# Performance work log

Hardware: AMD Instinct MI355X
Metric: run time of the kernel (lower is better)

The kernel has to match this reference:

```python
import jax, jax.numpy as jnp
import numpy as np

L, H, NH, HD, FF, S, B, V, NL = 2, 2048, 16, 128, 4096, 1024, 2, 32000, 4
R, SCALING, BLK = 2, 16.0 / 2.0, 64  # LoRA r=2, alpha=16 -> scaling 8; NF4 blocksize 64
NF4 = jnp.array([-1.0, -0.6961928009986877, -0.5250730514526367, -0.39491748809814453,
                 -0.28444138169288635, -0.18477343022823334, -0.09105003625154495, 0.0,
                 0.07958029955625534, 0.16093020141124725, 0.24611230194568634,
                 0.33791524171829224, 0.44070982933044434, 0.5626170039176941,
                 0.7229568362236023, 1.0], dtype=jnp.float32)

def dequant(codes, scales):
    # codes [out, in] int -> NF4 values; scales [out, in//BLK] absmax per 64-block
    return NF4[codes] * jnp.repeat(scales, BLK, axis=-1)

def qlin(x, codes, scales, A, Bm):
    # fused dequant + GEMM + LoRA low-rank update: x @ (Wd + s*B@A).T
    W = dequant(codes, scales)
    return x @ W.T + SCALING * ((x @ A.T) @ Bm.T)

def layer_norm(x, g, b):
    mu = jnp.mean(x, -1, keepdims=True)
    var = jnp.var(x, -1, keepdims=True)
    return (x - mu) * jax.lax.rsqrt(var + 1e-5) * g + b

def rope(x):  # x [B,S,NH,HD]
    half = HD // 2
    inv = 1.0 / (10000.0 ** (jnp.arange(half, dtype=jnp.float32) / half))
    ang = jnp.arange(S, dtype=jnp.float32)[:, None] * inv[None, :]
    cos = jnp.concatenate([jnp.cos(ang)] * 2, -1)[None, :, None, :]
    sin = jnp.concatenate([jnp.sin(ang)] * 2, -1)[None, :, None, :]
    x1, x2 = x[..., :half], x[..., half:]
    return x * cos + jnp.concatenate([-x2, x1], -1) * sin

def setup_inputs() -> dict:
    key = jax.random.key(0)
    it = iter(jax.random.split(key, 64))
    nrm = lambda shp, s: jax.random.normal(next(it), shp, jnp.float32) * s
    cod = lambda shp: jax.random.randint(next(it), shp, 0, 16, jnp.int32)
    scl = lambda shp: jax.random.uniform(next(it), shp, jnp.float32) * 0.02 + 1e-3
    lens = jax.random.randint(next(it), (B,), S // 2, S + 1)
    return dict(
        input_ids=jax.random.randint(next(it), (B, S), 0, V, jnp.int32),
        attention_mask=(jnp.arange(S)[None, :] < lens[:, None]).astype(jnp.int32),
        labels=jax.random.randint(next(it), (B,), 0, NL, jnp.int32),
        embed=nrm((V, H), 0.02),
        qkv_codes=cod((L, 3 * H, H)), qkv_scales=scl((L, 3 * H, H // BLK)),
        qkv_A=nrm((L, R, H), 0.01), qkv_B=nrm((L, 3 * H, R), 0.01),
        dense_codes=cod((L, H, H)), dense_scales=scl((L, H, H // BLK)),
        dense_A=nrm((L, R, H), 0.01), dense_B=nrm((L, H, R), 0.01),
        min_codes=cod((L, 2 * FF, H)), min_scales=scl((L, 2 * FF, H // BLK)),
        min_A=nrm((L, R, H), 0.01), min_B=nrm((L, 2 * FF, R), 0.01),
        mout_codes=cod((L, H, FF)), mout_scales=scl((L, H, FF // BLK)),
        mout_A=nrm((L, R, FF), 0.01), mout_B=nrm((L, H, R), 0.01),
        ln1_g=jnp.ones((L, H)), ln1_b=jnp.zeros((L, H)),
        ln2_g=jnp.ones((L, H)), ln2_b=jnp.zeros((L, H)),
        lnf_g=jnp.ones((H,)), lnf_b=jnp.zeros((H,)),
        classifier_w=nrm((NL, H), 0.01),
    )

def reference(input_ids, attention_mask, labels, embed, qkv_codes, qkv_scales, qkv_A, qkv_B,
              dense_codes, dense_scales, dense_A, dense_B, min_codes, min_scales, min_A, min_B,
              mout_codes, mout_scales, mout_A, mout_B, ln1_g, ln1_b, ln2_g, ln2_b,
              lnf_g, lnf_b, classifier_w):
    x = embed[input_ids]  # [B,S,H]
    mask = jnp.tril(jnp.ones((S, S), bool))[None, None] & (attention_mask[:, None, None, :] > 0)
    for l in range(L):
        h = layer_norm(x, ln1_g[l], ln1_b[l])
        qkv = qlin(h, qkv_codes[l], qkv_scales[l], qkv_A[l], qkv_B[l]).reshape(B, S, NH, 3 * HD)
        q, k, v = qkv[..., :HD], qkv[..., HD:2 * HD], qkv[..., 2 * HD:]
        q, k = rope(q), rope(k)
        scores = jnp.einsum('bqhd,bkhd->bhqk', q, k) / np.float32(np.sqrt(HD))
        probs = jax.nn.softmax(jnp.where(mask, scores, jnp.float32(-1e30)), -1)
        attn = jnp.einsum('bhqk,bkhd->bqhd', probs, v).reshape(B, S, H)
        x = x + qlin(attn, dense_codes[l], dense_scales[l], dense_A[l], dense_B[l])
        h2 = layer_norm(x, ln2_g[l], ln2_b[l])
        u = qlin(h2, min_codes[l], min_scales[l], min_A[l], min_B[l])  # [B,S,2*FF] packed SwiGLU
        g = jax.nn.silu(u[..., :FF]) * u[..., FF:]
        x = x + qlin(g, mout_codes[l], mout_scales[l], mout_A[l], mout_B[l])
    x = layer_norm(x, lnf_g, lnf_b)
    eos = x[jnp.arange(B), attention_mask.sum(1) - 1]  # last non-padded token hidden
    logits = eos @ classifier_w.T
    logp = jax.nn.log_softmax(logits, -1)
    loss = -jnp.mean(logp[jnp.arange(B), labels])
    return loss, logits
```

## Files before the change

kernel.cpp:

```cpp
#include <hip/hip_runtime.h>

typedef unsigned short u16;
typedef __attribute__((ext_vector_type(4))) float f32x4;
typedef __attribute__((ext_vector_type(8))) short short8;
typedef __attribute__((ext_vector_type(4))) short short4v;

constexpr int CL  = 2;
constexpr int CH  = 2048;
constexpr int CNH = 16;
constexpr int CHD = 128;
constexpr int CFF = 4096;
constexpr int CS  = 1024;
constexpr int CB  = 2;
constexpr int CNL = 4;
constexpr int CM  = CB * CS;
#define SCALING 8.0f

__device__ __constant__ float NF4TAB[16] = {
    -1.0f, -0.6961928009986877f, -0.5250730514526367f, -0.39491748809814453f,
    -0.28444138169288635f, -0.18477343022823334f, -0.09105003625154495f, 0.0f,
    0.07958029955625534f, 0.16093020141124725f, 0.24611230194568634f,
    0.33791524171829224f, 0.44070982933044434f, 0.5626170039176941f,
    0.7229568362236023f, 1.0f};

__device__ __forceinline__ u16 f2bf(float f) {
  union { float f; unsigned u; } v; v.f = f;
  unsigned r = v.u + 0x7fffu + ((v.u >> 16) & 1u);
  return (u16)(r >> 16);
}
__device__ __forceinline__ float bf2f(u16 u) {
  union { unsigned u; float f; } v; v.u = ((unsigned)u) << 16;
  return v.f;
}

__device__ __forceinline__ float blockReduceSum(float v) {
  __shared__ float sh[4];
  #pragma unroll
  for (int o = 32; o > 0; o >>= 1) v += __shfl_down(v, o);
  __syncthreads();
  if ((threadIdx.x & 63) == 0) sh[threadIdx.x >> 6] = v;
  __syncthreads();
  return sh[0] + sh[1] + sh[2] + sh[3];
}

__global__ void k_embed(const int* __restrict__ ids, const float* __restrict__ emb,
                        float* __restrict__ x) {
  int m = blockIdx.x;
  const float4* src = (const float4*)(emb + (size_t)ids[m] * CH);
  float4* dst = (float4*)(x + (size_t)m * CH);
  for (int i = threadIdx.x; i < CH / 4; i += 256) dst[i] = src[i];
}

__global__ void k_ln_xa(const float* __restrict__ x, const float* __restrict__ g,
                        const float* __restrict__ b, const float* __restrict__ A,
                        u16* __restrict__ o, float* __restrict__ xA) {
  int m = blockIdx.x, tid = threadIdx.x;
  const float* row = x + (size_t)m * CH;
  float s = 0.f, s2 = 0.f;
  for (int i = tid; i < CH / 4; i += 256) {
    float4 v = ((const float4*)row)[i];
    s += v.x + v.y + v.z + v.w;
    s2 += v.x * v.x + v.y * v.y + v.z * v.z + v.w * v.w;
  }
  s = blockReduceSum(s);
  s2 = blockReduceSum(s2);
  float mu = s / CH, var = s2 / CH - mu * mu;
  float rs = rsqrtf(var + 1e-5f);
  u16* orow = o + (size_t)m * CH;
  float s0 = 0.f, s1 = 0.f;
  for (int i = tid; i < CH / 4; i += 256) {
    float4 v = ((const float4*)row)[i];
    float4 gv = ((const float4*)g)[i];
    float4 bv = ((const float4*)b)[i];
    float4 a0 = ((const float4*)A)[i];
    float4 a1 = ((const float4*)(A + CH))[i];
    float h0 = (v.x - mu) * rs * gv.x + bv.x;
    float h1 = (v.y - mu) * rs * gv.y + bv.y;
    float h2 = (v.z - mu) * rs * gv.z + bv.z;
    float h3 = (v.w - mu) * rs * gv.w + bv.w;
    short4v ov = { (short)f2bf(h0), (short)f2bf(h1), (short)f2bf(h2), (short)f2bf(h3) };
    *(short4v*)(orow + i * 4) = ov;
    s0 += h0 * a0.x + h1 * a0.y + h2 * a0.z + h3 * a0.w;
    s1 += h0 * a1.x + h1 * a1.y + h2 * a1.z + h3 * a1.w;
  }
  s0 = blockReduceSum(s0);
  s1 = blockReduceSum(s1);
  if (tid == 0) { xA[2 * m] = s0; xA[2 * m + 1] = s1; }
}

__global__ void k_xa(const u16* __restrict__ xb, const float* __restrict__ A,
                     float* __restrict__ xA, int K) {
  int m = blockIdx.x, tid = threadIdx.x;
  const u16* row = xb + (size_t)m * K;
  float s0 = 0.f, s1 = 0.f;
  for (int c = tid; c < K / 8; c += 256) {
    short8 v = *(const short8*)(row + c * 8);
    #pragma unroll
    for (int e = 0; e < 8; ++e) {
      float f = bf2f((u16)v[e]);
      s0 += f * A[c * 8 + e];
      s1 += f * A[K + c * 8 + e];
    }
  }
  s0 = blockReduceSum(s0);
  s1 = blockReduceSum(s1);
  if (tid == 0) { xA[2 * m] = s0; xA[2 * m + 1] = s1; }
}

__global__ void k_dequant(const int* __restrict__ codes, const float* __restrict__ scales,
                          u16* __restrict__ w, int kshift, long total) {
  __shared__ float lut[16];
  if (threadIdx.x < 16) lut[threadIdx.x] = NF4TAB[threadIdx.x];
  __syncthreads();
  long base = ((long)blockIdx.x * 256 + threadIdx.x) * 8;
  if (base >= total) return;
  long n = base >> kshift;
  int k = (int)(base & ((1L << kshift) - 1));
  float sc = scales[(size_t)n * (1 << (kshift - 6)) + (k >> 6)];
  const int* cp = codes + base;
  short8 o;
  #pragma unroll
  for (int i = 0; i < 8; ++i) o[i] = (short)f2bf(lut[cp[i] & 15] * sc);
  *(short8*)(w + base) = o;
}

__global__ void k_ropetab(float* __restrict__ cosT, float* __restrict__ sinT) {
  int i = blockIdx.x * 256 + threadIdx.x;
  if (i >= CS * 64) return;
  int s = i >> 6, d = i & 63;
  float inv = powf(10000.0f, -(float)d / 64.0f);
  float a = (float)s * inv;
  cosT[i] = cosf(a);
  sinT[i] = sinf(a);
}

__global__ void k_rope(const u16* __restrict__ qkv, const float* __restrict__ cosT,
                       const float* __restrict__ sinT, u16* __restrict__ Qb,
                       u16* __restrict__ Kb) {
  int bid = blockIdx.x;
  int s = bid & (CS - 1);
  int z = bid >> 10;
  int b = z >> 4, h = z & 15;
  int d = threadIdx.x;
  const u16* base = qkv + ((size_t)(b * CS + s)) * (3 * CH) + h * (3 * CHD);
  int dh = d & 63;
  float c = cosT[s * 64 + dh], sn = sinT[s * 64 + dh];
  float sgn = (d < 64) ? -1.0f : 1.0f;
  float q = bf2f(base[d]),       qp = bf2f(base[d ^ 64]);
  float k = bf2f(base[CHD + d]), kp = bf2f(base[CHD + (d ^ 64)]);
  size_t oi = ((size_t)z * CS + s) * CHD + d;
  Qb[oi] = f2bf(q * c + sgn * qp * sn);
  Kb[oi] = f2bf(k * c + sgn * kp * sn);
}

__global__ void k_vtrans(const u16* __restrict__ qkv, u16* __restrict__ Vt) {
  __shared__ u16 tile[32][33];
  int z = blockIdx.z;
  int b = z >> 4, h = z & 15;
  int s0 = blockIdx.x * 32, d0 = blockIdx.y * 32;
  int tx = threadIdx.x, ty = threadIdx.y;
  #pragma unroll
  for (int i = 0; i < 32; i += 8)
    tile[ty + i][tx] =
        qkv[((size_t)(b * CS + s0 + ty + i)) * (3 * CH) + h * (3 * CHD) + 2 * CHD + d0 + tx];
  __syncthreads();
  #pragma unroll
  for (int i = 0; i < 32; i += 8)
    Vt[((size_t)z * CHD + d0 + ty + i) * CS + s0 + tx] = tile[tx][ty + i];
}

__global__ __launch_bounds__(256, 2) void k_flash(
    const u16* __restrict__ Qb, const u16* __restrict__ Kb, const u16* __restrict__ Vt,
    const int* __restrict__ amask, u16* __restrict__ out) {
  __shared__ u16 Ks[64 * 128];
  __shared__ u16 Vs[128 * 64];
  __shared__ float bias[CS];
  __shared__ u16 Ps[4][16][80];
  int bid = blockIdx.x;
  int qt = 15 - (bid >> 5);
  int z = bid & 31;
  int b = z >> 4, h = z & 15;
  int tid = threadIdx.x, lane = tid & 63, wid = tid >> 6;
  int lrow = lane & 15, lgrp = lane >> 4;
  const u16* Qz = Qb + (size_t)z * CS * CHD;
  const u16* Kz = Kb + (size_t)z * CS * CHD;
  const u16* Vz = Vt + (size_t)z * CHD * CS;

  for (int i = tid; i < CS; i += 256)
    bias[i] = amask[b * CS + i] ? 0.f : -1e30f;

  int qrow = qt * 64 + wid * 16 + lrow;
  short8 qf[4];
  #pragma unroll
  for (int kk = 0; kk < 4; ++kk)
    qf[kk] = *(const short8*)(Qz + (size_t)qrow * CHD + kk * 32 + lgrp * 8);

  float m_r[4], l_r[4];
  #pragma unroll
  for (int r = 0; r < 4; ++r) { m_r[r] = -3e38f; l_r[r] = 0.f; }
  f32x4 o_acc[8];
  #pragma unroll
  for (int dj = 0; dj < 8; ++dj) o_acc[dj] = (f32x4){0.f, 0.f, 0.f, 0.f};

  const float SCL = 0.08838834764831845f;

  for (int t = 0; t <= qt; ++t) {
    int k0 = t * 64;
    __syncthreads();
    #pragma unroll
    for (int it = 0; it < 4; ++it) {
      int c = it * 256 + tid;
      int key = c >> 4, ch = c & 15;
      short8 v = *(const short8*)(Kz + (size_t)(k0 + key) * CHD + ch * 8);
      *(short8*)((char*)Ks + key * 256 + ((ch * 16) ^ ((key & 7) << 4))) = v;
    }
    #pragma unroll
    for (int it = 0; it < 4; ++it) {
      int c = it * 256 + tid;
      int d = c >> 3, ch = c & 7;
      short8 v = *(const short8*)(Vz + (size_t)d * CS + k0 + ch * 8);
      *(short8*)((char*)Vs + d * 128 + ((ch * 16) ^ ((d & 7) << 4))) = v;
    }
    __syncthreads();

    f32x4 s_acc[4];
    #pragma unroll
    for (int nj = 0; nj < 4; ++nj) s_acc[nj] = (f32x4){0.f, 0.f, 0.f, 0.f};
    #pragma unroll
    for (int kk = 0; kk < 4; ++kk) {
      #pragma unroll
      for (int nj = 0; nj < 4; ++nj) {
        int key = nj * 16 + lrow;
        short8 kf = *(const short8*)((const char*)Ks + key * 256 +
                                     (((kk * 32 + lgrp * 8) * 2) ^ ((key & 7) << 4)));
        s_acc[nj] = __builtin_amdgcn_mfma_f32_16x16x32_bf16(qf[kk], kf, s_acc[nj], 0, 0, 0);
      }
    }

    bool diag = (t == qt);
    float p[4][4], mx[4];
    #pragma unroll
    for (int r = 0; r < 4; ++r) {
      int ql = wid * 16 + 4 * lgrp + r;
      float rm = -3e38f;
      #pragma unroll
      for (int nj = 0; nj < 4; ++nj) {
        int kl = nj * 16 + lrow;
        float v = s_acc[nj][r] * SCL + bias[k0 + kl];
        if (diag && kl > ql) v = -1e30f;
        p[nj][r] = v;
        rm = fmaxf(rm, v);
      }
      mx[r] = rm;
    }
    #pragma unroll
    for (int o = 1; o < 16; o <<= 1)
      #pragma unroll
      for (int r = 0; r < 4; ++r) mx[r] = fmaxf(mx[r], __shfl_xor(mx[r], o));
    float ps[4], alpha[4];
    #pragma unroll
    for (int r = 0; r < 4; ++r) {
      float mn = fmaxf(m_r[r], mx[r]);
      alpha[r] = __expf(m_r[r] - mn);
      m_r[r] = mn;
      float acc = 0.f;
      #pragma unroll
      for (int nj = 0; nj < 4; ++nj) {
        float e = __expf(p[nj][r] - mn);
        p[nj][r] = e;
        acc += e;
      }
      ps[r] = acc;
    }
    #pragma unroll
    for (int o = 1; o < 16; o <<= 1)
      #pragma unroll
      for (int r = 0; r < 4; ++r) ps[r] += __shfl_xor(ps[r], o);
    #pragma unroll
    for (int r = 0; r < 4; ++r) {
      l_r[r] = l_r[r] * alpha[r] + ps[r];
      #pragma unroll
      for (int dj = 0; dj < 8; ++dj) o_acc[dj][r] *= alpha[r];
    }

    #pragma unroll
    for (int r = 0; r < 4; ++r)
      #pragma unroll
      for (int nj = 0; nj < 4; ++nj)
        Ps[wid][4 * lgrp + r][nj * 16 + lrow] = f2bf(p[nj][r]);
    #pragma unroll
    for (int kk2 = 0; kk2 < 2; ++kk2) {
      short8 pa = *(const short8*)(&Ps[wid][lrow][kk2 * 32 + lgrp * 8]);
      #pragma unroll
      for (int dj = 0; dj < 8; ++dj) {
        int d = dj * 16 + lrow;
        short8 vf = *(const short8*)((const char*)Vs + d * 128 +
                                     (((kk2 * 32 + lgrp * 8) * 2) ^ ((d & 7) << 4)));
        o_acc[dj] = __builtin_amdgcn_mfma_f32_16x16x32_bf16(pa, vf, o_acc[dj], 0, 0, 0);
      }
    }
  }

  #pragma unroll
  for (int r = 0; r < 4; ++r) {
    float inv = 1.0f / l_r[r];
    int qg = qt * 64 + wid * 16 + 4 * lgrp + r;
    size_t rowoff = ((size_t)(b * CS + qg)) * CH + h * CHD;
    #pragma unroll
    for (int dj = 0; dj < 8; ++dj)
      out[rowoff + dj * 16 + lrow] = f2bf(o_acc[dj][r] * inv);
  }
}

__global__ void k_silu_xa(const u16* __restrict__ u, const float* __restrict__ A,
                          u16* __restrict__ g, float* __restrict__ xA) {
  int m = blockIdx.x, tid = threadIdx.x;
  const u16* urow = u + (size_t)m * (2 * CFF);
  u16* grow = g + (size_t)m * CFF;
  float s0 = 0.f, s1 = 0.f;
  for (int c = tid; c < CFF / 8; c += 256) {
    short8 va = *(const short8*)(urow + c * 8);
    short8 vb = *(const short8*)(urow + CFF + c * 8);
    short8 og;
    #pragma unroll
    for (int e = 0; e < 8; ++e) {
      float a = bf2f((u16)va[e]);
      float bb = bf2f((u16)vb[e]);
      float gg = (a / (1.0f + __expf(-a))) * bb;
      og[e] = (short)f2bf(gg);
      s0 += gg * A[c * 8 + e];
      s1 += gg * A[CFF + c * 8 + e];
    }
    *(short8*)(grow + c * 8) = og;
  }
  s0 = blockReduceSum(s0);
  s1 = blockReduceSum(s1);
  if (tid == 0) { xA[2 * m] = s0; xA[2 * m + 1] = s1; }
}

template <int OUT_BF16, int LORA, int RESID>
__global__ __launch_bounds__(256, 2) void k_gemm(
    const u16* __restrict__ Ag, const u16* __restrict__ Bg, void* __restrict__ Cout,
    const float* __restrict__ resid, const float* __restrict__ xA,
    const float* __restrict__ lB, int K, int N) {
  __shared__ u16 As[2][128 * 64];
  __shared__ u16 Bs[2][128 * 64];
  int tid = threadIdx.x, lane = tid & 63, wid = tid >> 6;
  int wm = wid >> 1, wn = wid & 1;
  int gx = gridDim.x, nwg = gx * gridDim.y;
  int bid = blockIdx.y * gx + blockIdx.x;
  int qq = nwg >> 3, rr = nwg & 7;
  int xcd = bid & 7, lid = bid >> 3;
  int swz = (xcd < rr ? xcd * (qq + 1) : rr * (qq + 1) + (xcd - rr) * qq) + lid;
  long bm = (long)(swz % gx) * 128, bn = (long)(swz / gx) * 128;

  f32x4 acc[4][4];
  #pragma unroll
  for (int i = 0; i < 4; ++i)
    #pragma unroll
    for (int j = 0; j < 4; ++j) acc[i][j] = (f32x4){0.f, 0.f, 0.f, 0.f};

  int lrow = lane >> 3;
  int lcol = ((lane & 7) ^ lrow) << 3;

  auto stage = [&](int buf, int k0) {
    #pragma unroll
    for (int it = 0; it < 4; ++it) {
      int sg = it * 4 + wid;
      long row = sg * 8 + lrow;
      __builtin_amdgcn_global_load_lds(
          (const __attribute__((address_space(1))) void*)(Ag + (size_t)(bm + row) * K + k0 + lcol),
          (__attribute__((address_space(3))) void*)(As[buf] + sg * 512), 16, 0, 0);
      __builtin_amdgcn_global_load_lds(
          (const __attribute__((address_space(1))) void*)(Bg + (size_t)(bn + row) * K + k0 + lcol),
          (__attribute__((address_space(3))) void*)(Bs[buf] + sg * 512), 16, 0, 0);
    }
  };

  stage(0, 0);
  __syncthreads();
  int nt = K >> 6;
  int cur = 0;
  for (int t = 0; t < nt; ++t) {
    if (t + 1 < nt) stage(cur ^ 1, (t + 1) * 64);
    #pragma unroll
    for (int kk = 0; kk < 2; ++kk) {
      short8 af[4], bfr[4];
      #pragma unroll
      for (int i = 0; i < 4; ++i) {
        int ar = wm * 64 + i * 16 + (lane & 15);
        int au = kk * 4 + (lane >> 4);
        af[i] = *(const short8*)(As[cur] + ar * 64 + ((au ^ (ar & 7)) << 3));
        int br = wn * 64 + i * 16 + (lane & 15);
        bfr[i] = *(const short8*)(Bs[cur] + br * 64 + ((au ^ (br & 7)) << 3));
      }
      #pragma unroll
      for (int i = 0; i < 4; ++i)
        #pragma unroll
        for (int j = 0; j < 4; ++j)
          acc[i][j] = __builtin_amdgcn_mfma_f32_16x16x32_bf16(af[i], bfr[j], acc[i][j], 0, 0, 0);
    }
    __syncthreads();
    cur ^= 1;
  }

  #pragma unroll
  for (int i = 0; i < 4; ++i) {
    #pragma unroll
    for (int r = 0; r < 4; ++r) {
      long m = bm + wm * 64 + i * 16 + ((lane >> 4) << 2) + r;
      float xa0 = 0.f, xa1 = 0.f;
      if (LORA) { xa0 = xA[2 * m]; xa1 = xA[2 * m + 1]; }
      #pragma unroll
      for (int j = 0; j < 4; ++j) {
        long n = bn + wn * 64 + j * 16 + (lane & 15);
        float v = acc[i][j][r];
        if (LORA) v += SCALING * (xa0 * lB[2 * n] + xa1 * lB[2 * n + 1]);
        if (RESID) v += resid[m * N + n];
        if (OUT_BF16)
          ((u16*)Cout)[m * N + n] = f2bf(v);
        else
          ((float*)Cout)[m * N + n] = v;
      }
    }
  }
}

__global__ void k_final(const float* __restrict__ x, const int* __restrict__ amask,
                        const int* __restrict__ labels, const float* __restrict__ g,
                        const float* __restrict__ bb, const float* __restrict__ cw,
                        float* __restrict__ out) {
  __shared__ float xr[CH];
  __shared__ float lg[CB][CNL];
  int tid = threadIdx.x;
  for (int b = 0; b < CB; ++b) {
    float fc = 0.f;
    for (int k = tid; k < CS; k += 256) fc += (amask[b * CS + k] != 0) ? 1.0f : 0.0f;
    int len = (int)(blockReduceSum(fc) + 0.5f);
    const float* row = x + ((size_t)b * CS + (len - 1)) * CH;
    float s = 0.f, s2 = 0.f;
    for (int k = tid; k < CH; k += 256) { float v = row[k]; s += v; s2 += v * v; }
    s = blockReduceSum(s);
    s2 = blockReduceSum(s2);
    float mu = s / CH, var = s2 / CH - mu * mu;
    float rs = rsqrtf(var + 1e-5f);
    for (int k = tid; k < CH; k += 256) xr[k] = (row[k] - mu) * rs * g[k] + bb[k];
    __syncthreads();
    for (int c = 0; c < CNL; ++c) {
      float p = 0.f;
      for (int k = tid; k < CH; k += 256) p += xr[k] * cw[c * CH + k];
      p = blockReduceSum(p);
      if (tid == 0) { lg[b][c] = p; out[1 + b * CNL + c] = p; }
    }
    __syncthreads();
  }
  if (tid == 0) {
    float loss = 0.f;
    for (int b = 0; b < CB; ++b) {
      float mx = -1e30f;
      for (int c = 0; c < CNL; ++c) mx = fmaxf(mx, lg[b][c]);
      float se = 0.f;
      for (int c = 0; c < CNL; ++c) se += expf(lg[b][c] - mx);
      float lse = mx + logf(se);
      loss -= (lg[b][labels[b]] - lse);
    }
    out[0] = loss / CB;
  }
}

static constexpr size_t X_OFF  = 0;
static constexpr size_t H_OFF  = X_OFF + (size_t)CM * CH * 4;
static constexpr size_t W_OFF  = H_OFF + (size_t)CM * CH * 2;
static constexpr size_t SC_OFF = W_OFF + (size_t)8192 * 2048 * 2;
static constexpr size_t PR_OFF = SC_OFF + (size_t)32 * CS * CS * 4;
static constexpr size_t XA_OFF = PR_OFF + (size_t)32 * CS * CS * 2;
static constexpr size_t CS_OFF = XA_OFF + (size_t)CM * 2 * 4;
static constexpr size_t SN_OFF = CS_OFF + (size_t)CS * 64 * 4;
static constexpr size_t WS_END = SN_OFF + (size_t)CS * 64 * 4;

extern "C" void kernel_launch(void* const* d_in, const int* in_sizes, int n_in,
                              void* d_out, int out_size, void* d_ws, size_t ws_size,
                              hipStream_t stream) {
  (void)in_sizes; (void)n_in; (void)out_size;
  if (ws_size < WS_END) return;

  const int*   ids          = (const int*)d_in[0];
  const int*   amask        = (const int*)d_in[1];
  const int*   labels       = (const int*)d_in[2];
  const float* emb          = (const float*)d_in[3];
  const int*   qkv_codes    = (const int*)d_in[4];
  const float* qkv_scales   = (const float*)d_in[5];
  const float* qkv_A        = (const float*)d_in[6];
  const float* qkv_B        = (const float*)d_in[7];
  const int*   dense_codes  = (const int*)d_in[8];
  const float* dense_scales = (const float*)d_in[9];
  const float* dense_A      = (const float*)d_in[10];
  const float* dense_B      = (const float*)d_in[11];
  const int*   min_codes    = (const int*)d_in[12];
  const float* min_scales   = (const float*)d_in[13];
  const float* min_A        = (const float*)d_in[14];
  const float* min_B        = (const float*)d_in[15];
  const int*   mout_codes   = (const int*)d_in[16];
  const float* mout_scales  = (const float*)d_in[17];
  const float* mout_A       = (const float*)d_in[18];
  const float* mout_B       = (const float*)d_in[19];
  const float* ln1_g        = (const float*)d_in[20];
  const float* ln1_b        = (const float*)d_in[21];
  const float* ln2_g        = (const float*)d_in[22];
  const float* ln2_b        = (const float*)d_in[23];
  const float* lnf_g        = (const float*)d_in[24];
  const float* lnf_b        = (const float*)d_in[25];
  const float* cw           = (const float*)d_in[26];

  char* ws = (char*)d_ws;
  float* x       = (float*)(ws + X_OFF);
  u16*   hbuf    = (u16*)(ws + H_OFF);
  u16*   wbuf    = (u16*)(ws + W_OFF);
  u16*   Qb      = (u16*)(ws + W_OFF);
  u16*   Kb      = (u16*)(ws + W_OFF + (size_t)32 * CS * CHD * 2);
  u16*   Vt      = (u16*)(ws + W_OFF + (size_t)64 * CS * CHD * 2);
  u16*   qkv_out = (u16*)(ws + SC_OFF);
  u16*   ubuf    = (u16*)(ws + SC_OFF);
  u16*   gbuf    = (u16*)(ws + PR_OFF);
  float* xA      = (float*)(ws + XA_OFF);
  float* cosT    = (float*)(ws + CS_OFF);
  float* sinT    = (float*)(ws + SN_OFF);

  k_ropetab<<<(CS * 64 + 255) / 256, 256, 0, stream>>>(cosT, sinT);
  k_embed<<<CM, 256, 0, stream>>>(ids, emb, x);

  for (int l = 0; l < CL; ++l) {
    k_ln_xa<<<CM, 256, 0, stream>>>(x, ln1_g + l * CH, ln1_b + l * CH,
                                    qkv_A + (size_t)l * 2 * CH, hbuf, xA);
    long nq = (long)3 * CH * CH;
    k_dequant<<<(int)(nq / 8 / 256), 256, 0, stream>>>(
        qkv_codes + (size_t)l * nq, qkv_scales + (size_t)l * 3 * CH * (CH / 64),
        wbuf, 11, nq);
    k_gemm<1, 1, 0><<<dim3(CM / 128, (3 * CH) / 128), 256, 0, stream>>>(
        hbuf, wbuf, qkv_out, nullptr, xA, qkv_B + (size_t)l * 3 * CH * 2, CH, 3 * CH);
    k_rope<<<32 * CS, 128, 0, stream>>>(qkv_out, cosT, sinT, Qb, Kb);
    k_vtrans<<<dim3(CS / 32, CHD / 32, 32), dim3(32, 8), 0, stream>>>(qkv_out, Vt);
    k_flash<<<512, 256, 0, stream>>>(Qb, Kb, Vt, amask, hbuf);
    k_xa<<<CM, 256, 0, stream>>>(hbuf, dense_A + (size_t)l * 2 * CH, xA, CH);
    long nd = (long)CH * CH;
    k_dequant<<<(int)(nd / 8 / 256), 256, 0, stream>>>(
        dense_codes + (size_t)l * nd, dense_scales + (size_t)l * CH * (CH / 64),
        wbuf, 11, nd);
    k_gemm<0, 1, 1><<<dim3(CM / 128, CH / 128), 256, 0, stream>>>(
        hbuf, wbuf, x, x, xA, dense_B + (size_t)l * CH * 2, CH, CH);

    k_ln_xa<<<CM, 256, 0, stream>>>(x, ln2_g + l * CH, ln2_b + l * CH,
                                    min_A + (size_t)l * 2 * CH, hbuf, xA);
    long nm = (long)2 * CFF * CH;
    k_dequant<<<(int)(nm / 8 / 256), 256, 0, stream>>>(
        min_codes + (size_t)l * nm, min_scales + (size_t)l * 2 * CFF * (CH / 64),
        wbuf, 11, nm);
    k_gemm<1, 1, 0><<<dim3(CM / 128, (2 * CFF) / 128), 256, 0, stream>>>(
        hbuf, wbuf, ubuf, nullptr, xA, min_B + (size_t)l * 2 * CFF * 2, CH, 2 * CFF);
    k_silu_xa<<<CM, 256, 0, stream>>>(ubuf, mout_A + (size_t)l * 2 * CFF, gbuf, xA);
    long no = (long)CH * CFF;
    k_dequant<<<(int)(no / 8 / 256), 256, 0, stream>>>(
        mout_codes + (size_t)l * no, mout_scales + (size_t)l * CH * (CFF / 64),
        wbuf, 12, no);
    k_gemm<0, 1, 1><<<dim3(CM / 128, CH / 128), 256, 0, stream>>>(
        gbuf, wbuf, x, x, xA, mout_B + (size_t)l * CH * 2, CFF, CH);
  }

  k_final<<<1, 256, 0, stream>>>(x, amask, labels, lnf_g, lnf_b, cw, (float*)d_out);
}
```

Before: 744.6 us.

## Replace GEMM with templated 4-stage pipelined kernel and 256x256 tiles for wide projections

```diff
diff --git a/kernel.cpp b/kernel.cpp
--- a/kernel.cpp
+++ b/kernel.cpp
@@ -338,82 +338,142 @@
   if (tid == 0) { xA[2 * m] = s0; xA[2 * m + 1] = s1; }
 }
 
-template <int OUT_BF16, int LORA, int RESID>
-__global__ __launch_bounds__(256, 2) void k_gemm(
+template <int BM, int BN, int TW, int WM, int WN, int OUT_BF16, int LORA, int RESID>
+__global__ __launch_bounds__(TW, 2) void k_gemm2(
     const u16* __restrict__ Ag, const u16* __restrict__ Bg, void* __restrict__ Cout,
     const float* __restrict__ resid, const float* __restrict__ xA,
     const float* __restrict__ lB, int K, int N) {
-  __shared__ u16 As[2][128 * 64];
-  __shared__ u16 Bs[2][128 * 64];
+  constexpr int WROWS = BM / WM, WCOLS = BN / WN;
+  constexpr int M_REP = WROWS / 16, N_REP = WCOLS / 16;
+  constexpr int MH = (M_REP > 4) ? 4 : M_REP;
+  constexpr int LA = (BM * 4) / TW;
+  constexpr int LB = (BN * 4) / TW;
+  __shared__ __align__(16) u16 As[4][BM * 32];
+  __shared__ __align__(16) u16 Bs[4][BN * 32];
   int tid = threadIdx.x, lane = tid & 63, wid = tid >> 6;
-  int wm = wid >> 1, wn = wid & 1;
+  int wm = wid / WN, wn = wid % WN;
   int gx = gridDim.x, nwg = gx * gridDim.y;
   int bid = blockIdx.y * gx + blockIdx.x;
   int qq = nwg >> 3, rr = nwg & 7;
   int xcd = bid & 7, lid = bid >> 3;
   int swz = (xcd < rr ? xcd * (qq + 1) : rr * (qq + 1) + (xcd - rr) * qq) + lid;
-  long bm = (long)(swz % gx) * 128, bn = (long)(swz / gx) * 128;
-
-  f32x4 acc[4][4];
-  #pragma unroll
-  for (int i = 0; i < 4; ++i)
-    #pragma unroll
-    for (int j = 0; j < 4; ++j) acc[i][j] = (f32x4){0.f, 0.f, 0.f, 0.f};
-
-  int lrow = lane >> 3;
-  int lcol = ((lane & 7) ^ lrow) << 3;
-
-  auto stage = [&](int buf, int k0) {
-    #pragma unroll
-    for (int it = 0; it < 4; ++it) {
-      int sg = it * 4 + wid;
-      long row = sg * 8 + lrow;
+  long bm = (long)(swz % gx) * BM, bn = (long)(swz / gx) * BN;
+
+  f32x4 acc[M_REP][N_REP];
+  #pragma unroll
+  for (int i = 0; i < M_REP; ++i)
+    #pragma unroll
+    for (int j = 0; j < N_REP; ++j) acc[i][j] = (f32x4){0.f, 0.f, 0.f, 0.f};
+
+  auto stageA = [&](int buf, int t) {
+    int k0 = t * 32;
+    #pragma unroll
+    for (int i = 0; i < LA; ++i) {
+      int fa = i * TW + tid;
+      int r = fa >> 2, p = fa & 3;
+      int g = (p + 4 - ((r >> 1) & 3)) & 3;
       __builtin_amdgcn_global_load_lds(
-          (const __attribute__((address_space(1))) void*)(Ag + (size_t)(bm + row) * K + k0 + lcol),
-          (__attribute__((address_space(3))) void*)(As[buf] + sg * 512), 16, 0, 0);
+          (const __attribute__((address_space(1))) void*)(Ag + (size_t)(bm + r) * K + k0 + g * 8),
+          (__attribute__((address_space(3))) void*)(&As[buf][fa * 8]), 16, 0, 0);
+    }
+  };
+  auto stageB = [&](int buf, int t) {
+    int k0 = t * 32;
+    #pragma unroll
+    for (int i = 0; i < LB; ++i) {
+      int fa = i * TW + tid;
+      int r = fa >> 2, p = fa & 3;
+      int g = (p + 4 - ((r >> 1) & 3)) & 3;
       __builtin_amdgcn_global_load_lds(
-          (const __attribute__((address_space(1))) void*)(Bg + (size_t)(bn + row) * K + k0 + lcol),
-          (__attribute__((address_space(3))) void*)(Bs[buf] + sg * 512), 16, 0, 0);
+          (const __attribute__((address_space(1))) void*)(Bg + (size_t)(bn + r) * K + k0 + g * 8),
+          (__attribute__((address_space(3))) void*)(&Bs[buf][fa * 8]), 16, 0, 0);
     }
   };
 
-  stage(0, 0);
-  __syncthreads();
-  int nt = K >> 6;
-  int cur = 0;
-  for (int t = 0; t < nt; ++t) {
-    if (t + 1 < nt) stage(cur ^ 1, (t + 1) * 64);
-    #pragma unroll
-    for (int kk = 0; kk < 2; ++kk) {
-      short8 af[4], bfr[4];
-      #pragma unroll
-      for (int i = 0; i < 4; ++i) {
-        int ar = wm * 64 + i * 16 + (lane & 15);
-        int au = kk * 4 + (lane >> 4);
-        af[i] = *(const short8*)(As[cur] + ar * 64 + ((au ^ (ar & 7)) << 3));
-        int br = wn * 64 + i * 16 + (lane & 15);
-        bfr[i] = *(const short8*)(Bs[cur] + br * 64 + ((au ^ (br & 7)) << 3));
-      }
-      #pragma unroll
-      for (int i = 0; i < 4; ++i)
+  int NT = K >> 5;
+  stageA(0, 0); stageB(0, 0);
+  stageA(1, 1); stageB(1, 1);
+
+  int kg = lane >> 4, lr = lane & 15;
+  for (int t = 0; t < NT; ++t) {
+    int buf = t & 3;
+    if (t + 1 < NT) asm volatile("s_waitcnt vmcnt(4)" ::: "memory");
+    else            asm volatile("s_waitcnt vmcnt(0)" ::: "memory");
+    __builtin_amdgcn_s_barrier();
+
+    short8 bfr[N_REP];
+    #pragma unroll
+    for (int j = 0; j < N_REP; ++j) {
+      int r = wn * WCOLS + j * 16 + lr;
+      int slot = (kg + ((r >> 1) & 3)) & 3;
+      bfr[j] = *(const short8*)(&Bs[buf][r * 32 + slot * 8]);
+    }
+
+    if constexpr (M_REP == MH) {
+      if (t + 2 < NT) { stageA((t + 2) & 3, t + 2); stageB((t + 2) & 3, t + 2); }
+      short8 af[MH];
+      #pragma unroll
+      for (int i = 0; i < MH; ++i) {
+        int r = wm * WROWS + i * 16 + lr;
+        int slot = (kg + ((r >> 1) & 3)) & 3;
+        af[i] = *(const short8*)(&As[buf][r * 32 + slot * 8]);
+      }
+      __builtin_amdgcn_s_setprio(1);
+      #pragma unroll
+      for (int i = 0; i < MH; ++i)
         #pragma unroll
-        for (int j = 0; j < 4; ++j)
+        for (int j = 0; j < N_REP; ++j)
           acc[i][j] = __builtin_amdgcn_mfma_f32_16x16x32_bf16(af[i], bfr[j], acc[i][j], 0, 0, 0);
-    }
-    __syncthreads();
-    cur ^= 1;
-  }
-
-  #pragma unroll
-  for (int i = 0; i < 4; ++i) {
+      __builtin_amdgcn_s_setprio(0);
+    } else {
+      if (t + 2 < NT) stageA((t + 2) & 3, t + 2);
+      {
+        short8 af[MH];
+        #pragma unroll
+        for (int i = 0; i < MH; ++i) {
+          int r = wm * WROWS + i * 16 + lr;
+          int slot = (kg + ((r >> 1) & 3)) & 3;
+          af[i] = *(const short8*)(&As[buf][r * 32 + slot * 8]);
+        }
+        __builtin_amdgcn_s_setprio(1);
+        #pragma unroll
+        for (int i = 0; i < MH; ++i)
+          #pragma unroll
+          for (int j = 0; j < N_REP; ++j)
+            acc[i][j] = __builtin_amdgcn_mfma_f32_16x16x32_bf16(af[i], bfr[j], acc[i][j], 0, 0, 0);
+        __builtin_amdgcn_s_setprio(0);
+      }
+      __builtin_amdgcn_s_barrier();
+      if (t + 2 < NT) stageB((t + 2) & 3, t + 2);
+      {
+        short8 af[M_REP - MH];
+        #pragma unroll
+        for (int i = 0; i < M_REP - MH; ++i) {
+          int r = wm * WROWS + (MH + i) * 16 + lr;
+          int slot = (kg + ((r >> 1) & 3)) & 3;
+          af[i] = *(const short8*)(&As[buf][r * 32 + slot * 8]);
+        }
+        __builtin_amdgcn_s_setprio(1);
+        #pragma unroll
+        for (int i = 0; i < M_REP - MH; ++i)
+          #pragma unroll
+          for (int j = 0; j < N_REP; ++j)
+            acc[MH + i][j] = __builtin_amdgcn_mfma_f32_16x16x32_bf16(af[i], bfr[j], acc[MH + i][j], 0, 0, 0);
+        __builtin_amdgcn_s_setprio(0);
+      }
+    }
+  }
+
+  #pragma unroll
+  for (int i = 0; i < M_REP; ++i) {
     #pragma unroll
     for (int r = 0; r < 4; ++r) {
-      long m = bm + wm * 64 + i * 16 + ((lane >> 4) << 2) + r;
+      long m = bm + wm * WROWS + i * 16 + ((lane >> 4) << 2) + r;
       float xa0 = 0.f, xa1 = 0.f;
       if (LORA) { xa0 = xA[2 * m]; xa1 = xA[2 * m + 1]; }
       #pragma unroll
-      for (int j = 0; j < 4; ++j) {
-        long n = bn + wn * 64 + j * 16 + (lane & 15);
+      for (int j = 0; j < N_REP; ++j) {
+        long n = bn + wn * WCOLS + j * 16 + (lane & 15);
         float v = acc[i][j][r];
         if (LORA) v += SCALING * (xa0 * lB[2 * n] + xa1 * lB[2 * n + 1]);
         if (RESID) v += resid[m * N + n];
@@ -536,7 +596,7 @@
     k_dequant<<<(int)(nq / 8 / 256), 256, 0, stream>>>(
         qkv_codes + (size_t)l * nq, qkv_scales + (size_t)l * 3 * CH * (CH / 64),
         wbuf, 11, nq);
-    k_gemm<1, 1, 0><<<dim3(CM / 128, (3 * CH) / 128), 256, 0, stream>>>(
+    k_gemm2<256, 256, 512, 2, 4, 1, 1, 0><<<dim3(CM / 256, (3 * CH) / 256), 512, 0, stream>>>(
         hbuf, wbuf, qkv_out, nullptr, xA, qkv_B + (size_t)l * 3 * CH * 2, CH, 3 * CH);
     k_rope<<<32 * CS, 128, 0, stream>>>(qkv_out, cosT, sinT, Qb, Kb);
     k_vtrans<<<dim3(CS / 32, CHD / 32, 32), dim3(32, 8), 0, stream>>>(qkv_out, Vt);
@@ -546,7 +606,7 @@
     k_dequant<<<(int)(nd / 8 / 256), 256, 0, stream>>>(
         dense_codes + (size_t)l * nd, dense_scales + (size_t)l * CH * (CH / 64),
         wbuf, 11, nd);
-    k_gemm<0, 1, 1><<<dim3(CM / 128, CH / 128), 256, 0, stream>>>(
+    k_gemm2<128, 128, 256, 2, 2, 0, 1, 1><<<dim3(CM / 128, CH / 128), 256, 0, stream>>>(
         hbuf, wbuf, x, x, xA, dense_B + (size_t)l * CH * 2, CH, CH);
 
     k_ln_xa<<<CM, 256, 0, stream>>>(x, ln2_g + l * CH, ln2_b + l * CH,
@@ -555,14 +615,14 @@
     k_dequant<<<(int)(nm / 8 / 256), 256, 0, stream>>>(
         min_codes + (size_t)l * nm, min_scales + (size_t)l * 2 * CFF * (CH / 64),
         wbuf, 11, nm);
-    k_gemm<1, 1, 0><<<dim3(CM / 128, (2 * CFF) / 128), 256, 0, stream>>>(
+    k_gemm2<256, 256, 512, 2, 4, 1, 1, 0><<<dim3(CM / 256, (2 * CFF) / 256), 512, 0, stream>>>(
         hbuf, wbuf, ubuf, nullptr, xA, min_B + (size_t)l * 2 * CFF * 2, CH, 2 * CFF);
     k_silu_xa<<<CM, 256, 0, stream>>>(ubuf, mout_A + (size_t)l * 2 * CFF, gbuf, xA);
     long no = (long)CH * CFF;
     k_dequant<<<(int)(no / 8 / 256), 256, 0, stream>>>(
         mout_codes + (size_t)l * no, mout_scales + (size_t)l * CH * (CFF / 64),
         wbuf, 12, no);
-    k_gemm<0, 1, 1><<<dim3(CM / 128, CH / 128), 256, 0, stream>>>(
+    k_gemm2<128, 128, 256, 2, 2, 0, 1, 1><<<dim3(CM / 128, CH / 128), 256, 0, stream>>>(
         gbuf, wbuf, x, x, xA, mout_B + (size_t)l * CH * 2, CFF, CH);
   }
 
```

Result: slower. 917.5 us (+23.2%).
